# Kernel optimization log

Measured on AMD Instinct MI355X. Metric: run time of the kernel, lower is better.

## Reference

```python
import jax, jax.numpy as jnp
import numpy as np

B, T, D = 16, 4096, 512
N_SLOTS = 64


def setup_inputs() -> dict:
    key = jax.random.key(0)
    ks = jax.random.split(key, 7)
    s = 1.0 / np.sqrt(D)  # keep tanh out of deep saturation, like orthogonal*0.9 init
    return {
        "x_seq": jax.random.normal(ks[0], (B, T, D), jnp.float32),
        "h_tape": jax.random.normal(ks[1], (B, N_SLOTS, D), jnp.float32) * 0.1,
        "h_work": jax.random.normal(ks[2], (B, D), jnp.float32) * 0.1,
        "W_h": jax.random.normal(ks[3], (D, D), jnp.float32) * s,
        "W_x": jax.random.normal(ks[4], (D, D), jnp.float32) * s,
        "b_h": jnp.zeros((D,), jnp.float32),
        "W_write": jax.random.normal(ks[5], (D, D), jnp.float32) * s,
    }


def reference(x_seq, h_tape, h_work, W_h, W_x, b_h, W_write):
    """Dual-memory Elman recurrence.

    Per step t:
      read_t  = softmax(h_tape @ h_work / sqrt(D)) @ h_tape   (content-based tape read)
      h_work  = tanh(W_h h_work + W_x x_t + read_t + b_h)
      tape write: slot (t mod n_slots) <- W_write h_work      (FIFO tape write)
    Returns (h_work_out [B,T,D], h_tape_final [B,S,D], last h_work [B,D]).
    """
    scale = jnp.asarray(1.0 / np.sqrt(D), x_seq.dtype)

    def step(carry, inp):
        tape, h = carry
        x_t, t = inp
        scores = jnp.einsum("bsd,bd->bs", tape, h) * scale        # [B,S]
        attn = jax.nn.softmax(scores, axis=-1)
        read = jnp.einsum("bs,bsd->bd", attn, tape)               # [B,D]
        h_new = jnp.tanh(h @ W_h.T + x_t @ W_x.T + read + b_h)    # [B,D]
        w_vec = h_new @ W_write.T                                 # [B,D]
        slot = t % N_SLOTS
        tape = jax.lax.dynamic_update_slice(tape, w_vec[:, None, :], (0, slot, 0))
        return (tape, h_new), h_new

    xs = (jnp.swapaxes(x_seq, 0, 1), jnp.arange(x_seq.shape[1]))
    (tape_f, _), h_seq = jax.lax.scan(step, (h_tape, h_work), xs)
    h_work_out = jnp.swapaxes(h_seq, 0, 1)  # [B,T,D]
    return h_work_out, tape_f, h_work_out[:, -1]
```

## Files before the change

kernel.cpp:

```cpp
#include <hip/hip_runtime.h>
#include <cstddef>

#define B_SZ   16
#define T_SZ   4096
#define D_SZ   512
#define NSLOT  64
#define NW     16
#define RPW    32
#define WP     516
#define TP     36
#define FPAD   64
#define SCALE  0.044194173824159216f

__device__ __align__(16) float g_ps[B_SZ * NW * NSLOT];
__device__ __align__(16) float g_hx[B_SZ * NW * RPW];
__device__ int g_sf[B_SZ * NW * FPAD];
__device__ int g_hf[B_SZ * NW * FPAD];

#define AL(p)    __hip_atomic_load((p),  __ATOMIC_RELAXED, __HIP_MEMORY_SCOPE_AGENT)
#define AS(p,v)  __hip_atomic_store((p), (v), __ATOMIC_RELAXED, __HIP_MEMORY_SCOPE_AGENT)
#define VMCNT0() __asm__ __volatile__("s_waitcnt vmcnt(0)" ::: "memory")

__global__ __launch_bounds__(256)
void xw_gemm_kernel(const float* __restrict__ X, const float* __restrict__ Wx,
                    const float* __restrict__ bh, float* __restrict__ out)
{
    __shared__ float As[16][68];
    __shared__ float Bs[16][68];
    const int m0 = blockIdx.x * 64;
    const int n0 = blockIdx.y * 64;
    const int tid = threadIdx.x;
    const int tr = tid >> 4, tc = tid & 15;
    const int lrow = tid >> 2;
    const int lkk  = (tid & 3) * 4;

    float acc[4][4] = {};

    for (int k0 = 0; k0 < D_SZ; k0 += 16) {
        float4 av = *(const float4*)(X  + (size_t)(m0 + lrow) * D_SZ + k0 + lkk);
        float4 bv = *(const float4*)(Wx + (size_t)(n0 + lrow) * D_SZ + k0 + lkk);
        As[lkk+0][lrow] = av.x; As[lkk+1][lrow] = av.y;
        As[lkk+2][lrow] = av.z; As[lkk+3][lrow] = av.w;
        Bs[lkk+0][lrow] = bv.x; Bs[lkk+1][lrow] = bv.y;
        Bs[lkk+2][lrow] = bv.z; Bs[lkk+3][lrow] = bv.w;
        __syncthreads();
        #pragma unroll
        for (int kk = 0; kk < 16; ++kk) {
            float a[4], b[4];
            #pragma unroll
            for (int i = 0; i < 4; ++i) a[i] = As[kk][tr*4+i];
            #pragma unroll
            for (int j = 0; j < 4; ++j) b[j] = Bs[kk][tc*4+j];
            #pragma unroll
            for (int i = 0; i < 4; ++i)
                #pragma unroll
                for (int j = 0; j < 4; ++j)
                    acc[i][j] = fmaf(a[i], b[j], acc[i][j]);
        }
        __syncthreads();
    }
    #pragma unroll
    for (int i = 0; i < 4; ++i) {
        const int m = m0 + tr*4 + i;
        const int n = n0 + tc*4;
        float4 o;
        o.x = acc[i][0] + bh[n+0];
        o.y = acc[i][1] + bh[n+1];
        o.z = acc[i][2] + bh[n+2];
        o.w = acc[i][3] + bh[n+3];
        *(float4*)(out + (size_t)m * D_SZ + n) = o;
    }
}

__global__ __launch_bounds__(256, 1)
void recurrence_mw(const float* __restrict__ tape0, const float* __restrict__ h0,
                   const float* __restrict__ W_h, const float* __restrict__ W_w,
                   float* __restrict__ out)
{
    __shared__ float Wh_s[RPW][WP];
    __shared__ float Ww_s[RPW][WP];
    __shared__ float tp[NSLOT][TP];
    __shared__ float hh[D_SZ];
    __shared__ float ps_l[NSLOT];
    __shared__ float attn[NSLOT];
    __shared__ float zmv[RPW];
    __shared__ float rp8[8][RPW];

    const int blk = blockIdx.x;
    const int xcd = blk & 7;
    const int jj0 = blk >> 3;
    const int b   = xcd * 2 + (jj0 & 1);
    const int w   = jj0 >> 1;
    const int R0  = w * RPW;
    const int tid = threadIdx.x;
    const int fb  = b * NW;

    for (int i = tid; i < RPW * (D_SZ / 4); i += 256) {
        const int r = i >> 7, c = (i & 127) * 4;
        *(float4*)&Wh_s[r][c] = *(const float4*)(W_h + (size_t)(R0 + r) * D_SZ + c);
        *(float4*)&Ww_s[r][c] = *(const float4*)(W_w + (size_t)(R0 + r) * D_SZ + c);
    }
    for (int i = tid; i < NSLOT * RPW; i += 256) {
        const int s = i >> 5, jc = i & 31;
        tp[s][jc] = tape0[((size_t)b * NSLOT + s) * D_SZ + R0 + jc];
    }
    for (int i = tid; i < D_SZ; i += 256) hh[i] = h0[(size_t)b * D_SZ + i];
    __syncthreads();

    float* outb = out + (size_t)b * T_SZ * D_SZ;

    const int sA = tid >> 2, qA = tid & 3;
    const int g16 = tid >> 4, sj = tid & 15;
    const int jB = tid & 31, sg = tid >> 5;

    for (int t = 0; t < T_SZ; ++t) {
        float xwv = 0.f;
        if (tid < RPW) xwv = outb[(size_t)t * D_SZ + R0 + tid];

        {
            float4 t0 = *(const float4*)&tp[sA][qA * 8];
            float4 t1 = *(const float4*)&tp[sA][qA * 8 + 4];
            float4 ha = *(const float4*)&hh[R0 + qA * 8];
            float4 hb = *(const float4*)&hh[R0 + qA * 8 + 4];
            float acc = t0.x*ha.x + t0.y*ha.y + t0.z*ha.z + t0.w*ha.w
                      + t1.x*hb.x + t1.y*hb.y + t1.z*hb.z + t1.w*hb.w;
            acc += __shfl_xor(acc, 1);
            acc += __shfl_xor(acc, 2);
            if (qA == 0) ps_l[sA] = acc;
        }
        __syncthreads();

        if (tid < NSLOT) AS(&g_ps[(fb + w) * NSLOT + tid], ps_l[tid]);
        if (tid == 0) { VMCNT0(); AS(&g_sf[(fb + w) * FPAD], t + 1); }

        {
            float4 hr[8];
            #pragma unroll
            for (int i = 0; i < 8; ++i) hr[i] = *(const float4*)&hh[4 * sj + 64 * i];
            #pragma unroll
            for (int p = 0; p < 2; ++p) {
                const int row = g16 + p * 16;
                float acc = 0.f;
                #pragma unroll
                for (int i = 0; i < 8; ++i) {
                    float4 wv = *(const float4*)&Wh_s[row][4 * sj + 64 * i];
                    acc = fmaf(wv.x, hr[i].x, acc);
                    acc = fmaf(wv.y, hr[i].y, acc);
                    acc = fmaf(wv.z, hr[i].z, acc);
                    acc = fmaf(wv.w, hr[i].w, acc);
                }
                acc += __shfl_xor(acc, 1);
                acc += __shfl_xor(acc, 2);
                acc += __shfl_xor(acc, 4);
                acc += __shfl_xor(acc, 8);
                if (sj == 0) zmv[row] = acc;
            }
        }

        if (tid >= 64 && tid < 64 + NW) {
            while (AL(&g_sf[(fb + (tid - 64)) * FPAD]) != t + 1)
                __builtin_amdgcn_s_sleep(1);
        }
        __syncthreads();

        {
            float acc = 0.f;
            #pragma unroll
            for (int k = 0; k < 4; ++k)
                acc += AL(&g_ps[(fb + qA * 4 + k) * NSLOT + sA]);
            acc += __shfl_xor(acc, 1);
            acc += __shfl_xor(acc, 2);
            if (qA == 0) ps_l[sA] = acc * SCALE;
        }
        __syncthreads();

        if (tid < 64) {
            const float v = ps_l[tid];
            float m = v;
            #pragma unroll
            for (int o = 32; o; o >>= 1) m = fmaxf(m, __shfl_xor(m, o));
            const float e = __expf(v - m);
            float s = e;
            #pragma unroll
            for (int o = 32; o; o >>= 1) s += __shfl_xor(s, o);
            attn[tid] = e / s;
        }
        __syncthreads();

        {
            float acc = 0.f;
            #pragma unroll
            for (int s8 = 0; s8 < 8; ++s8)
                acc = fmaf(attn[sg * 8 + s8], tp[sg * 8 + s8][jB], acc);
            rp8[sg][jB] = acc;
        }
        __syncthreads();

        if (tid < RPW) {
            const float rr = rp8[0][tid] + rp8[1][tid] + rp8[2][tid] + rp8[3][tid]
                           + rp8[4][tid] + rp8[5][tid] + rp8[6][tid] + rp8[7][tid];
            const float v = tanhf(zmv[tid] + rr + xwv);
            outb[(size_t)t * D_SZ + R0 + tid] = v;
            AS(&g_hx[(fb + w) * RPW + tid], v);
        }
        if (tid == 0) { VMCNT0(); AS(&g_hf[(fb + w) * FPAD], t + 1); }
        if (tid >= 64 && tid < 64 + NW) {
            while (AL(&g_hf[(fb + (tid - 64)) * FPAD]) != t + 1)
                __builtin_amdgcn_s_sleep(1);
        }
        __syncthreads();

        {
            const int i0 = tid * 2;
            hh[i0]     = AL(&g_hx[fb * RPW + i0]);
            hh[i0 + 1] = AL(&g_hx[fb * RPW + i0 + 1]);
        }
        __syncthreads();

        {
            const int slot = t & (NSLOT - 1);
            float4 hr[8];
            #pragma unroll
            for (int i = 0; i < 8; ++i) hr[i] = *(const float4*)&hh[4 * sj + 64 * i];
            #pragma unroll
            for (int p = 0; p < 2; ++p) {
                const int row = g16 + p * 16;
                float acc = 0.f;
                #pragma unroll
                for (int i = 0; i < 8; ++i) {
                    float4 wv = *(const float4*)&Ww_s[row][4 * sj + 64 * i];
                    acc = fmaf(wv.x, hr[i].x, acc);
                    acc = fmaf(wv.y, hr[i].y, acc);
                    acc = fmaf(wv.z, hr[i].z, acc);
                    acc = fmaf(wv.w, hr[i].w, acc);
                }
                acc += __shfl_xor(acc, 1);
                acc += __shfl_xor(acc, 2);
                acc += __shfl_xor(acc, 4);
                acc += __shfl_xor(acc, 8);
                if (sj == 0) tp[slot][row] = acc;
            }
        }
        __syncthreads();
    }

    float* tout = out + (size_t)B_SZ * T_SZ * D_SZ + (size_t)b * NSLOT * D_SZ;
    for (int i = tid; i < NSLOT * RPW; i += 256) {
        const int s = i >> 5, jc = i & 31;
        tout[(size_t)s * D_SZ + R0 + jc] = tp[s][jc];
    }
    if (tid < RPW) {
        float* lout = out + (size_t)B_SZ * T_SZ * D_SZ
                          + (size_t)B_SZ * NSLOT * D_SZ + (size_t)b * D_SZ;
        lout[R0 + tid] = hh[R0 + tid];
    }
}

extern "C" void kernel_launch(void* const* d_in, const int* in_sizes, int n_in,
                              void* d_out, int out_size, void* d_ws, size_t ws_size,
                              hipStream_t stream)
{
    const float* x_seq   = (const float*)d_in[0];
    const float* h_tape  = (const float*)d_in[1];
    const float* h_work  = (const float*)d_in[2];
    const float* W_h     = (const float*)d_in[3];
    const float* W_x     = (const float*)d_in[4];
    const float* b_h     = (const float*)d_in[5];
    const float* W_write = (const float*)d_in[6];
    float* out = (float*)d_out;

    dim3 g1(T_SZ * B_SZ / 64, D_SZ / 64);
    xw_gemm_kernel<<<g1, 256, 0, stream>>>(x_seq, W_x, b_h, out);

    recurrence_mw<<<B_SZ * NW, 256, 0, stream>>>(h_tape, h_work, W_h, W_write, out);
}
```

Baseline: 18.53 ms.

## Replace flag-based cross-block sync with tagged 64-bit value-plus-step mailboxes

Packs each exchanged float together with its step tag into one 64-bit word, so consumer threads poll the data itself. This removes the separate flag stores, the vmcnt waits and one barrier per exchange. It also preloads the W_write rows into registers before the h-exchange wait, so the LDS reads overlap the spin. In exchange, the exchange buffers carry twice the bytes, every thread now polls global memory instead of a few, and register pressure rises.

```diff
diff --git a/kernel.cpp b/kernel.cpp
--- a/kernel.cpp
+++ b/kernel.cpp
@@ -9,17 +9,17 @@
 #define RPW    32
 #define WP     516
 #define TP     36
-#define FPAD   64
 #define SCALE  0.044194173824159216f
 
-__device__ __align__(16) float g_ps[B_SZ * NW * NSLOT];
-__device__ __align__(16) float g_hx[B_SZ * NW * RPW];
-__device__ int g_sf[B_SZ * NW * FPAD];
-__device__ int g_hf[B_SZ * NW * FPAD];
+__device__ __align__(8) unsigned long long g_ps2[B_SZ * NW * NSLOT];
+__device__ __align__(8) unsigned long long g_hx2[B_SZ * D_SZ];
 
 #define AL(p)    __hip_atomic_load((p),  __ATOMIC_RELAXED, __HIP_MEMORY_SCOPE_AGENT)
 #define AS(p,v)  __hip_atomic_store((p), (v), __ATOMIC_RELAXED, __HIP_MEMORY_SCOPE_AGENT)
-#define VMCNT0() __asm__ __volatile__("s_waitcnt vmcnt(0)" ::: "memory")
+
+__device__ __forceinline__ unsigned long long pk(float v, unsigned tag) {
+    return ((unsigned long long)tag << 32) | (unsigned long long)__float_as_uint(v);
+}
 
 __global__ __launch_bounds__(256)
 void xw_gemm_kernel(const float* __restrict__ X, const float* __restrict__ Wx,
@@ -95,6 +95,9 @@
     const int tid = threadIdx.x;
     const int fb  = b * NW;
 
+    if (tid < NSLOT) AS(&g_ps2[(size_t)(fb + w) * NSLOT + tid], 0ULL);
+    if (tid < RPW)   AS(&g_hx2[(size_t)b * D_SZ + R0 + tid], 0ULL);
+
     for (int i = tid; i < RPW * (D_SZ / 4); i += 256) {
         const int r = i >> 7, c = (i & 127) * 4;
         *(float4*)&Wh_s[r][c] = *(const float4*)(W_h + (size_t)(R0 + r) * D_SZ + c);
@@ -114,6 +117,7 @@
     const int jB = tid & 31, sg = tid >> 5;
 
     for (int t = 0; t < T_SZ; ++t) {
+        const unsigned tg = (unsigned)(t + 1);
         float xwv = 0.f;
         if (tid < RPW) xwv = outb[(size_t)t * D_SZ + R0 + tid];
 
@@ -130,8 +134,8 @@
         }
         __syncthreads();
 
-        if (tid < NSLOT) AS(&g_ps[(fb + w) * NSLOT + tid], ps_l[tid]);
-        if (tid == 0) { VMCNT0(); AS(&g_sf[(fb + w) * FPAD], t + 1); }
+        if (tid < NSLOT)
+            AS(&g_ps2[(size_t)(fb + w) * NSLOT + tid], pk(ps_l[tid], tg));
 
         {
             float4 hr[8];
@@ -157,17 +161,18 @@
             }
         }
 
-        if (tid >= 64 && tid < 64 + NW) {
-            while (AL(&g_sf[(fb + (tid - 64)) * FPAD]) != t + 1)
+        {
+            const unsigned long long* pp = &g_ps2[(size_t)(fb + qA * 4) * NSLOT + sA];
+            unsigned long long v0, v1, v2, v3;
+            for (;;) {
+                v0 = AL(pp + 0 * NSLOT); v1 = AL(pp + 1 * NSLOT);
+                v2 = AL(pp + 2 * NSLOT); v3 = AL(pp + 3 * NSLOT);
+                if ((unsigned)(v0 >> 32) == tg && (unsigned)(v1 >> 32) == tg &&
+                    (unsigned)(v2 >> 32) == tg && (unsigned)(v3 >> 32) == tg) break;
                 __builtin_amdgcn_s_sleep(1);
-        }
-        __syncthreads();
-
-        {
-            float acc = 0.f;
-            #pragma unroll
-            for (int k = 0; k < 4; ++k)
-                acc += AL(&g_ps[(fb + qA * 4 + k) * NSLOT + sA]);
+            }
+            float acc = __uint_as_float((unsigned)v0) + __uint_as_float((unsigned)v1)
+                      + __uint_as_float((unsigned)v2) + __uint_as_float((unsigned)v3);
             acc += __shfl_xor(acc, 1);
             acc += __shfl_xor(acc, 2);
             if (qA == 0) ps_l[sA] = acc * SCALE;
@@ -201,19 +206,27 @@
                            + rp8[4][tid] + rp8[5][tid] + rp8[6][tid] + rp8[7][tid];
             const float v = tanhf(zmv[tid] + rr + xwv);
             outb[(size_t)t * D_SZ + R0 + tid] = v;
-            AS(&g_hx[(fb + w) * RPW + tid], v);
-        }
-        if (tid == 0) { VMCNT0(); AS(&g_hf[(fb + w) * FPAD], t + 1); }
-        if (tid >= 64 && tid < 64 + NW) {
-            while (AL(&g_hf[(fb + (tid - 64)) * FPAD]) != t + 1)
+            AS(&g_hx2[(size_t)b * D_SZ + R0 + tid], pk(v, tg));
+        }
+
+        float4 wv0[8], wv1[8];
+        #pragma unroll
+        for (int i = 0; i < 8; ++i) {
+            wv0[i] = *(const float4*)&Ww_s[g16][4 * sj + 64 * i];
+            wv1[i] = *(const float4*)&Ww_s[g16 + 16][4 * sj + 64 * i];
+        }
+
+        {
+            const int d0 = tid * 2;
+            const unsigned long long* hp = &g_hx2[(size_t)b * D_SZ + d0];
+            unsigned long long v0, v1;
+            for (;;) {
+                v0 = AL(hp); v1 = AL(hp + 1);
+                if ((unsigned)(v0 >> 32) == tg && (unsigned)(v1 >> 32) == tg) break;
                 __builtin_amdgcn_s_sleep(1);
-        }
-        __syncthreads();
-
-        {
-            const int i0 = tid * 2;
-            hh[i0]     = AL(&g_hx[fb * RPW + i0]);
-            hh[i0 + 1] = AL(&g_hx[fb * RPW + i0 + 1]);
+            }
+            hh[d0]     = __uint_as_float((unsigned)v0);
+            hh[d0 + 1] = __uint_as_float((unsigned)v1);
         }
         __syncthreads();
 
@@ -222,23 +235,25 @@
             float4 hr[8];
             #pragma unroll
             for (int i = 0; i < 8; ++i) hr[i] = *(const float4*)&hh[4 * sj + 64 * i];
-            #pragma unroll
-            for (int p = 0; p < 2; ++p) {
-                const int row = g16 + p * 16;
-                float acc = 0.f;
-                #pragma unroll
-                for (int i = 0; i < 8; ++i) {
-                    float4 wv = *(const float4*)&Ww_s[row][4 * sj + 64 * i];
-                    acc = fmaf(wv.x, hr[i].x, acc);
-                    acc = fmaf(wv.y, hr[i].y, acc);
-                    acc = fmaf(wv.z, hr[i].z, acc);
-                    acc = fmaf(wv.w, hr[i].w, acc);
-                }
-                acc += __shfl_xor(acc, 1);
-                acc += __shfl_xor(acc, 2);
-                acc += __shfl_xor(acc, 4);
-                acc += __shfl_xor(acc, 8);
-                if (sj == 0) tp[slot][row] = acc;
+            float a0 = 0.f, a1 = 0.f;
+            #pragma unroll
+            for (int i = 0; i < 8; ++i) {
+                a0 = fmaf(wv0[i].x, hr[i].x, a0);
+                a0 = fmaf(wv0[i].y, hr[i].y, a0);
+                a0 = fmaf(wv0[i].z, hr[i].z, a0);
+                a0 = fmaf(wv0[i].w, hr[i].w, a0);
+                a1 = fmaf(wv1[i].x, hr[i].x, a1);
+                a1 = fmaf(wv1[i].y, hr[i].y, a1);
+                a1 = fmaf(wv1[i].z, hr[i].z, a1);
+                a1 = fmaf(wv1[i].w, hr[i].w, a1);
+            }
+            a0 += __shfl_xor(a0, 1); a1 += __shfl_xor(a1, 1);
+            a0 += __shfl_xor(a0, 2); a1 += __shfl_xor(a1, 2);
+            a0 += __shfl_xor(a0, 4); a1 += __shfl_xor(a1, 4);
+            a0 += __shfl_xor(a0, 8); a1 += __shfl_xor(a1, 8);
+            if (sj == 0) {
+                tp[slot][g16]      = a0;
+                tp[slot][g16 + 16] = a1;
             }
         }
         __syncthreads();
```

Measured after the change: 17.55 ms. 1.06x faster.
